# Optimization experiments

Measured on AMD Instinct MI355X. Metric: run time of the kernel, lower is better.

The kernel has to match this reference:

```python
import jax, jax.numpy as jnp
import numpy as np

B, H, W, C = 8, 56, 56, 384
HEADS, K, PAD = 12, 3, 1


def setup_inputs() -> dict:
    key = jax.random.key(0)
    k1, k2, k3, k4 = jax.random.split(key, 4)
    s = 1.0 / np.sqrt(C).astype(np.float32)
    return {
        "x": jax.random.normal(k1, (B, H, W, C), jnp.float32),
        "Wv": jax.random.normal(k2, (C, C), jnp.float32) * s,
        "Wa": jax.random.normal(k3, (K ** 4 * HEADS, C), jnp.float32) * s,
        "Wo": jax.random.normal(k4, (C, C), jnp.float32) * s,
    }


def reference(x, Wv, Wa, Wo):
    b, h, w, c = x.shape
    heads, k, pad = HEADS, K, PAD
    d = c // heads
    k2 = k * k
    n = h * w  # stride=1 -> pooled grid == input grid, AvgPool2d(1,1) is identity

    # value projection then unfold into k x k local windows (overlap via padding)
    v = jnp.einsum('bhwc,oc->bhwo', x, Wv)
    vp = jnp.pad(v, ((0, 0), (pad, pad), (pad, pad), (0, 0)))
    # (b, h, w, k2, c): window position p = i*k + j
    patches = jnp.stack([vp[:, i:i + h, j:j + w] for i in range(k) for j in range(k)], axis=3)
    v_unf = patches.reshape(b, n, k2, heads, d)

    a = jnp.einsum('bhwc,oc->bhwo', x, Wa).reshape(b, n, heads, k2, k2)
    attn = jax.nn.softmax(a * (d ** -0.5), axis=-1)  # (b, n, heads, k2, k2)

    # weighted combination of window values
    out = jnp.einsum('bnhpq,bnqhd->bnphd', attn, v_unf).reshape(b, h, w, k2, c)

    # fold: overlap-add each window position back onto the padded canvas
    canvas = jnp.zeros((b, h + 2 * pad, w + 2 * pad, c), x.dtype)
    p = 0
    for i in range(k):
        for j in range(k):
            canvas = canvas.at[:, i:i + h, j:j + w].add(out[:, :, :, p])
            p += 1
    y = canvas[:, pad:pad + h, pad:pad + w]

    return jnp.einsum('bhwc,oc->bhwo', y, Wo)
```

## Files before the change

### kernel.cpp

```cpp
#include <hip/hip_runtime.h>
#include <hip/hip_bf16.h>

#define B_ 8
#define H_ 56
#define W_ 56
#define C_ 384
#define HEADS_ 12
#define NPIX (B_*H_*W_)
#define NPAD 1408
#define KDIM 384

typedef unsigned short u16;
typedef __attribute__((ext_vector_type(4))) float f32x4;
typedef __attribute__((ext_vector_type(8))) short bf16x8;
typedef __attribute__((ext_vector_type(8))) unsigned short u16x8;

#define GLDS16(g, l)                                                            \
    __builtin_amdgcn_global_load_lds(                                           \
        (const __attribute__((address_space(1))) void*)(g),                     \
        (__attribute__((address_space(3))) void*)(l), 16, 0, 0)

__device__ __forceinline__ float bf2f(u16 u) {
    union { unsigned int uu; float f; } cv; cv.uu = ((unsigned)u) << 16; return cv.f;
}
__device__ __forceinline__ u16 f2bf(float f) {
    __hip_bfloat16 hb = __float2bfloat16(f);
    return *reinterpret_cast<u16*>(&hb);
}

__global__ void pack_kernel(const float* __restrict__ x, const float* __restrict__ Wv,
                            const float* __restrict__ Wa, const float* __restrict__ Wo,
                            u16* __restrict__ xb, __hip_bfloat16* __restrict__ wcat,
                            __hip_bfloat16* __restrict__ wob) {
    const int NX8 = NPIX * C_ / 8;
    const int NW = NPAD * KDIM;
    const int NO = C_ * C_;
    const int total = NX8 + NW + NO;
    for (int idx = blockIdx.x * blockDim.x + threadIdx.x; idx < total;
         idx += gridDim.x * blockDim.x) {
        if (idx < NX8) {
            float4 a = ((const float4*)x)[idx * 2];
            float4 b = ((const float4*)x)[idx * 2 + 1];
            u16x8 o;
            o[0] = f2bf(a.x); o[1] = f2bf(a.y); o[2] = f2bf(a.z); o[3] = f2bf(a.w);
            o[4] = f2bf(b.x); o[5] = f2bf(b.y); o[6] = f2bf(b.z); o[7] = f2bf(b.w);
            ((u16x8*)xb)[idx] = o;
        } else if (idx < NX8 + NW) {
            int t = idx - NX8;
            int o = t / KDIM;
            float v = 0.f;
            if (o < 384) v = Wv[t];
            else if (o < 1356) v = Wa[t - 147456];
            wcat[t] = __float2bfloat16(v);
        } else {
            int t = idx - NX8 - NW;
            wob[t] = __float2bfloat16(Wo[t]);
        }
    }
}


#define STAGE(buf_, kt_) do {                                                        \
    _Pragma("unroll") for (int c = 0; c < 4; ++c) {                                  \
        int rowA = (wid * 4 + c) * 8 + srow;                                         \
        int scol = (sslot ^ (rowA & 7)) * 8;                                         \
        GLDS16(&A[(size_t)(bm * 128 + rowA) * K + (kt_) + scol],                     \
               &As[buf_][(wid * 4 + c) * 512]);                                      \
        GLDS16(&Bw[(size_t)(bn * 128 + rowA) * K + (kt_) + scol],                    \
               &Bs[buf_][(wid * 4 + c) * 512]);                                      \
    } } while (0)

template<int OUT_BF16>
__global__ __launch_bounds__(256) void gemm_bt(const u16* __restrict__ A, const u16* __restrict__ Bw,
                                               void* __restrict__ Cout, int N, int K,
                                               int gridN, int q, int r) {
    __shared__ u16 As[2][128 * 64];
    __shared__ u16 Bs[2][128 * 64];
    const int bid = blockIdx.x;
    const int xcd = bid & 7, ii = bid >> 3;
    const int logical = (xcd < r) ? xcd * (q + 1) + ii : r * (q + 1) + (xcd - r) * q + ii;
    const int bm = logical / gridN, bn = logical - bm * gridN;
    const int tid = threadIdx.x;
    const int lane = tid & 63, wid = tid >> 6;
    const int wm = wid >> 1, wn = wid & 1;
    const int fr = lane & 15;
    const int kg = lane >> 4;
    const int srow = lane >> 3;
    const int sslot = lane & 7;
    const int NT = K >> 6;
    f32x4 acc[4][4] = {};

    STAGE(0, 0);
    __syncthreads();
    for (int t = 0; t < NT; ++t) {
        const int cur = t & 1;
        if (t + 1 < NT) STAGE((t + 1) & 1, (t + 1) * 64);
#pragma unroll
        for (int ks = 0; ks < 2; ++ks) {
            bf16x8 af[4], bfr[4];
#pragma unroll
            for (int m = 0; m < 4; ++m) {
                int row = wm * 64 + m * 16 + fr;
                int slot = (ks * 4 + kg) ^ (row & 7);
                af[m] = *(const bf16x8*)(&As[cur][row * 64 + slot * 8]);
            }
#pragma unroll
            for (int n = 0; n < 4; ++n) {
                int row = wn * 64 + n * 16 + fr;
                int slot = (ks * 4 + kg) ^ (row & 7);
                bfr[n] = *(const bf16x8*)(&Bs[cur][row * 64 + slot * 8]);
            }
#pragma unroll
            for (int m = 0; m < 4; ++m)
#pragma unroll
                for (int n = 0; n < 4; ++n)
                    acc[m][n] = __builtin_amdgcn_mfma_f32_16x16x32_bf16(af[m], bfr[n], acc[m][n], 0, 0, 0);
        }
        __syncthreads();
    }
    const int r0 = bm * 128 + wm * 64 + kg * 4;
    const int c0 = bn * 128 + wn * 64 + fr;
#pragma unroll
    for (int m = 0; m < 4; ++m)
#pragma unroll
        for (int n = 0; n < 4; ++n)
#pragma unroll
            for (int j = 0; j < 4; ++j) {
                size_t off = (size_t)(r0 + m * 16 + j) * N + (c0 + n * 16);
                if (OUT_BF16) ((__hip_bfloat16*)Cout)[off] = __float2bfloat16(acc[m][n][j]);
                else          ((float*)Cout)[off] = acc[m][n][j];
            }
}

__global__ __launch_bounds__(384) void attn_fold(const __hip_bfloat16* __restrict__ va,
                                                 __hip_bfloat16* __restrict__ yb) {
    __shared__ float wls[8][300];
    const int tid = threadIdx.x;
    const int pix0 = blockIdx.x * 8;
    const u16* vap = (const u16*)va;

    if (tid < 96) {
        const int pixL = tid / 12, h = tid - pixL * 12;
        const int pix = pix0 + pixL;
        const int b = pix / 3136, rs = pix - b * 3136;
        const int r = rs / 56, s = rs - r * 56;
        float w[25];
#pragma unroll
        for (int t = 0; t < 25; ++t) w[t] = 0.f;
        const float SC = 0.17677669529663687f;
#pragma unroll
        for (int i = 0; i < 3; ++i) {
            int cy = r + 1 - i;
            if ((unsigned)cy >= (unsigned)H_) continue;
#pragma unroll
            for (int j = 0; j < 3; ++j) {
                int cx = s + 1 - j;
                if ((unsigned)cx >= (unsigned)W_) continue;
                const u16* ap = vap + (size_t)(b * 3136 + cy * 56 + cx) * NPAD + C_ + h * 81 + (i * 3 + j) * 9;
                float aq[9];
                float mx = -1e30f;
#pragma unroll
                for (int qq = 0; qq < 9; ++qq) { aq[qq] = bf2f(ap[qq]); mx = fmaxf(mx, aq[qq]); }
                float ssum = 0.f;
#pragma unroll
                for (int qq = 0; qq < 9; ++qq) { aq[qq] = __expf((aq[qq] - mx) * SC); ssum += aq[qq]; }
                float inv = 1.f / ssum;
#pragma unroll
                for (int qi = 0; qi < 3; ++qi)
#pragma unroll
                    for (int qj = 0; qj < 3; ++qj)
                        w[(qi - i + 2) * 5 + (qj - j + 2)] += aq[qi * 3 + qj] * inv;
            }
        }
#pragma unroll
        for (int t = 0; t < 25; ++t) wls[pixL][t * 12 + h] = w[t];
    }
    __syncthreads();

    const int g = tid / 48, t = tid - g * 48;
    const int c0 = t * 8, hh = t >> 2;
    const int pix = pix0 + g;
    const int b = pix / 3136, rs = pix - b * 3136;
    const int r = rs / 56, s = rs - r * 56;
    float acc[8];
#pragma unroll
    for (int e = 0; e < 8; ++e) acc[e] = 0.f;
    const float* wp = &wls[g][hh];
#pragma unroll
    for (int dy = -2; dy <= 2; ++dy) {
        int py = r + dy;
        if ((unsigned)py >= (unsigned)H_) continue;
#pragma unroll
        for (int dx = -2; dx <= 2; ++dx) {
            int px = s + dx;
            if ((unsigned)px >= (unsigned)W_) continue;
            float w = wp[((dy + 2) * 5 + (dx + 2)) * 12];
            u16x8 v = *(const u16x8*)(vap + (size_t)(b * 3136 + py * 56 + px) * NPAD + c0);
#pragma unroll
            for (int e = 0; e < 8; ++e) acc[e] += w * bf2f(v[e]);
        }
    }
    u16x8 o;
#pragma unroll
    for (int e = 0; e < 8; ++e) o[e] = f2bf(acc[e]);
    *(u16x8*)((u16*)yb + (size_t)pix * C_ + c0) = o;
}

extern "C" void kernel_launch(void* const* d_in, const int* in_sizes, int n_in,
                              void* d_out, int out_size, void* d_ws, size_t ws_size,
                              hipStream_t stream) {
    const float* x  = (const float*)d_in[0];
    const float* Wv = (const float*)d_in[1];
    const float* Wa = (const float*)d_in[2];
    const float* Wo = (const float*)d_in[3];
    char* ws = (char*)d_ws;
    u16*            xb   = (u16*)(ws);
    __hip_bfloat16* wcat = (__hip_bfloat16*)(ws + 19267584);
    __hip_bfloat16* wob  = (__hip_bfloat16*)(ws + 20348928);
    __hip_bfloat16* va   = (__hip_bfloat16*)(ws + 20643840);
    __hip_bfloat16* yb   = (__hip_bfloat16*)(ws + 91291648);

    hipLaunchKernelGGL(pack_kernel, dim3(2048), dim3(256), 0, stream,
                       x, Wv, Wa, Wo, xb, wcat, wob);

    {
        int gridN = NPAD / 128, nwg = (NPIX / 128) * gridN;
        int q = nwg / 8, r = nwg % 8;
        hipLaunchKernelGGL(HIP_KERNEL_NAME(gemm_bt<1>), dim3(nwg), dim3(256), 0, stream,
                           (const u16*)xb, (const u16*)wcat, (void*)va, NPAD, KDIM, gridN, q, r);
    }
    hipLaunchKernelGGL(attn_fold, dim3(NPIX / 8), dim3(384), 0, stream, va, yb);
    {
        int gridN = C_ / 128, nwg = (NPIX / 128) * gridN;
        int q = nwg / 8, r = nwg % 8;
        hipLaunchKernelGGL(HIP_KERNEL_NAME(gemm_bt<0>), dim3(nwg), dim3(256), 0, stream,
                           (const u16*)yb, (const u16*)wob, d_out, C_, KDIM, gridN, q, r);
    }
}
```

Before: 133.2 us.

## Rework attn_fold to process 32 pixels per block with wider per-thread channel tiles

The attention-fold kernel now handles 32 pixels per workgroup instead of 8, so all 384 threads take part in the softmax-weight phase (one pixel-head pair each) rather than only 96. In the fold phase each thread accumulates 32 channels of one pixel, using four 16-byte loads per neighbor instead of one. Block indices are interleaved across the batch dimension. The intent is to stop leaving most threads idle during the weight phase and to cut per-block overhead. The cost is fewer blocks, higher register pressure from 32 accumulators, and less coalesced loads per thread.

```diff
diff --git a/kernel.cpp b/kernel.cpp
--- a/kernel.cpp
+++ b/kernel.cpp
@@ -134,15 +134,17 @@
 
 __global__ __launch_bounds__(384) void attn_fold(const __hip_bfloat16* __restrict__ va,
                                                  __hip_bfloat16* __restrict__ yb) {
-    __shared__ float wls[8][300];
+    __shared__ float wls[32][300];
     const int tid = threadIdx.x;
-    const int pix0 = blockIdx.x * 8;
+    const int bid = blockIdx.x;
+    const int b = bid & 7;
+    const int bi = bid >> 3;
+    const int pix0base = bi * 32;
     const u16* vap = (const u16*)va;
 
-    if (tid < 96) {
+    {
         const int pixL = tid / 12, h = tid - pixL * 12;
-        const int pix = pix0 + pixL;
-        const int b = pix / 3136, rs = pix - b * 3136;
+        const int rs = pix0base + pixL;
         const int r = rs / 56, s = rs - r * 56;
         float w[25];
 #pragma unroll
@@ -177,33 +179,42 @@
     }
     __syncthreads();
 
-    const int g = tid / 48, t = tid - g * 48;
-    const int c0 = t * 8, hh = t >> 2;
-    const int pix = pix0 + g;
-    const int b = pix / 3136, rs = pix - b * 3136;
-    const int r = rs / 56, s = rs - r * 56;
-    float acc[8];
-#pragma unroll
-    for (int e = 0; e < 8; ++e) acc[e] = 0.f;
-    const float* wp = &wls[g][hh];
-#pragma unroll
-    for (int dy = -2; dy <= 2; ++dy) {
-        int py = r + dy;
-        if ((unsigned)py >= (unsigned)H_) continue;
-#pragma unroll
-        for (int dx = -2; dx <= 2; ++dx) {
-            int px = s + dx;
-            if ((unsigned)px >= (unsigned)W_) continue;
-            float w = wp[((dy + 2) * 5 + (dx + 2)) * 12];
-            u16x8 v = *(const u16x8*)(vap + (size_t)(b * 3136 + py * 56 + px) * NPAD + c0);
-#pragma unroll
-            for (int e = 0; e < 8; ++e) acc[e] += w * bf2f(v[e]);
-        }
-    }
-    u16x8 o;
-#pragma unroll
-    for (int e = 0; e < 8; ++e) o[e] = f2bf(acc[e]);
-    *(u16x8*)((u16*)yb + (size_t)pix * C_ + c0) = o;
+    {
+        const int pixL = tid / 12, k = tid - pixL * 12;
+        const int c0 = k * 32;
+        const int rs = pix0base + pixL;
+        const int r = rs / 56, s = rs - r * 56;
+        float acc[32];
+#pragma unroll
+        for (int e = 0; e < 32; ++e) acc[e] = 0.f;
+        const float* wp = &wls[pixL][k];
+#pragma unroll
+        for (int dy = -2; dy <= 2; ++dy) {
+            int py = r + dy;
+            if ((unsigned)py >= (unsigned)H_) continue;
+#pragma unroll
+            for (int dx = -2; dx <= 2; ++dx) {
+                int px = s + dx;
+                if ((unsigned)px >= (unsigned)W_) continue;
+                float w = wp[((dy + 2) * 5 + (dx + 2)) * 12];
+                const u16* vb = vap + (size_t)(b * 3136 + py * 56 + px) * NPAD + c0;
+#pragma unroll
+                for (int v4 = 0; v4 < 4; ++v4) {
+                    u16x8 v = *(const u16x8*)(vb + v4 * 8);
+#pragma unroll
+                    for (int e = 0; e < 8; ++e) acc[v4 * 8 + e] += w * bf2f(v[e]);
+                }
+            }
+        }
+        u16* yp = (u16*)yb + (size_t)(b * 3136 + rs) * C_ + c0;
+#pragma unroll
+        for (int v4 = 0; v4 < 4; ++v4) {
+            u16x8 o;
+#pragma unroll
+            for (int e = 0; e < 8; ++e) o[e] = f2bf(acc[v4 * 8 + e]);
+            *(u16x8*)(yp + v4 * 8) = o;
+        }
+    }
 }
 
 extern "C" void kernel_launch(void* const* d_in, const int* in_sizes, int n_in,
@@ -229,7 +240,7 @@
         hipLaunchKernelGGL(HIP_KERNEL_NAME(gemm_bt<1>), dim3(nwg), dim3(256), 0, stream,
                            (const u16*)xb, (const u16*)wcat, (void*)va, NPAD, KDIM, gridN, q, r);
     }
-    hipLaunchKernelGGL(attn_fold, dim3(NPIX / 8), dim3(384), 0, stream, va, yb);
+    hipLaunchKernelGGL(attn_fold, dim3(NPIX / 32), dim3(384), 0, stream, va, yb);
     {
         int gridN = C_ / 128, nwg = (NPIX / 128) * gridN;
         int q = nwg / 8, r = nwg % 8;
```

Measured after the change: 135.0 us. No clear change (+1.3%).
